# Kernel optimization log

Hardware: AMD Instinct MI355X
Metric: run time of the kernel (lower is better)

Reference implementation:

```python
import jax, jax.numpy as jnp
import numpy as np
from jax import lax

NUM_EMBEDDINGS = 4096
EMBEDDING_DIM = 512
COMMITMENT_COST = 0.1
N_TOKENS = 32768


def setup_inputs() -> dict:
    key = jax.random.key(0)
    kx, kc = jax.random.split(key)
    x = jax.random.normal(kx, (N_TOKENS, EMBEDDING_DIM), dtype=jnp.float32)
    # torch init: uniform_(-1/num_embeddings, 1/num_embeddings)
    lim = 1.0 / NUM_EMBEDDINGS
    codebook = jax.random.uniform(kc, (NUM_EMBEDDINGS, EMBEDDING_DIM),
                                  dtype=jnp.float32, minval=-lim, maxval=lim)
    return {"x": x, "codebook": codebook}


def reference(x, codebook):
    # x: [N, D] (already flat); codebook: [K, D]
    flat = x.reshape(-1, EMBEDDING_DIM)
    distances = (jnp.sum(flat * flat, axis=1, keepdims=True)
                 + jnp.sum(codebook * codebook, axis=1)
                 - 2.0 * jnp.matmul(flat, codebook.T))
    encoding_indices = jnp.argmin(distances, axis=1)  # [N]
    quantized = codebook[encoding_indices].reshape(x.shape)  # gather [N, D]
    e_latent_loss = jnp.mean((lax.stop_gradient(quantized) - x) ** 2)
    q_latent_loss = jnp.mean((quantized - lax.stop_gradient(x)) ** 2)
    loss = q_latent_loss + COMMITMENT_COST * e_latent_loss
    # straight-through estimator
    quantized_st = x + lax.stop_gradient(quantized - x)
    return quantized_st, loss, encoding_indices[:, None]
```

## Files before the change

### kernel.cpp

```cpp
#include <hip/hip_runtime.h>

#define N_TOK 32768
#define DIM 512
#define K_CODES 4096
#define KP 1536
#define CMARG 8e-5f

typedef __attribute__((ext_vector_type(8))) short bf16x8;
typedef __attribute__((ext_vector_type(4))) float f32x4;

__device__ __forceinline__ unsigned short f2bf(float f) {
    unsigned u = __float_as_uint(f);
    return (unsigned short)((u + 0x7FFFu + ((u >> 16) & 1u)) >> 16);
}
__device__ __forceinline__ float bf2f(unsigned short h) {
    return __uint_as_float((unsigned)h << 16);
}
__device__ __forceinline__ void gld16(const void* g, void* l) {
    __builtin_amdgcn_global_load_lds((const __attribute__((address_space(1))) void*)g,
                                     (__attribute__((address_space(3))) void*)l, 16, 0, 0);
}

__global__ __launch_bounds__(256) void vq_x2(const float* __restrict__ X, float* __restrict__ X2) {
    int n = blockIdx.x * 256 + threadIdx.x;
    const float* xr = X + (size_t)n * DIM;
    float blk[4];
    #pragma unroll
    for (int b = 0; b < 4; ++b) {
        const float* p = xr + b * 128;
        float lane[16];
        #pragma unroll
        for (int L = 0; L < 16; ++L) {
            float s[8];
            #pragma unroll
            for (int r = 0; r < 8; ++r) { float x = p[r * 16 + L]; s[r] = __fmul_rn(x, x); }
            float a01 = __fadd_rn(s[0], s[1]);
            float a23 = __fadd_rn(s[2], s[3]);
            float a45 = __fadd_rn(s[4], s[5]);
            float a67 = __fadd_rn(s[6], s[7]);
            lane[L] = __fadd_rn(__fadd_rn(a01, a23), __fadd_rn(a45, a67));
        }
        float t[8];
        #pragma unroll
        for (int L = 0; L < 8; ++L) t[L] = __fadd_rn(lane[L], lane[L + 8]);
        float u[4];
        #pragma unroll
        for (int L = 0; L < 4; ++L) u[L] = __fadd_rn(t[L], t[L + 4]);
        blk[b] = __fadd_rn(__fadd_rn(u[0], u[2]), __fadd_rn(u[1], u[3]));
    }
    X2[n] = __fadd_rn(__fadd_rn(blk[0], blk[1]), __fadd_rn(blk[2], blk[3]));
}

__global__ __launch_bounds__(256) void vq_split(const float* __restrict__ X, const float* __restrict__ CB,
        unsigned short* __restrict__ Ah, unsigned short* __restrict__ Al,
        unsigned short* __restrict__ Eh, unsigned short* __restrict__ El) {
    size_t idx = ((size_t)blockIdx.x * 256 + threadIdx.x) * 8;
    const size_t XE = (size_t)N_TOK * DIM;
    const float* src;
    unsigned short *dh, *dl;
    size_t off;
    if (idx < XE) { src = X + idx; dh = Ah; dl = Al; off = idx; }
    else          { src = CB + (idx - XE); dh = Eh; dl = El; off = idx - XE; }
    float4 v0 = *(const float4*)src;
    float4 v1 = *(const float4*)(src + 4);
    float xv[8] = {v0.x, v0.y, v0.z, v0.w, v1.x, v1.y, v1.z, v1.w};
    union { unsigned short u[8]; uint4 v; } H, L;
    #pragma unroll
    for (int u = 0; u < 8; ++u) {
        unsigned short hb = f2bf(xv[u]);
        H.u[u] = hb;
        L.u[u] = f2bf(__fadd_rn(xv[u], -bf2f(hb)));
    }
    *(uint4*)(dh + off) = H.v;
    *(uint4*)(dl + off) = L.v;
}

__global__ __launch_bounds__(256, 2) void vq_gemm(
        const unsigned short* __restrict__ Ah, const unsigned short* __restrict__ Al,
        const unsigned short* __restrict__ Eh, const unsigned short* __restrict__ El,
        float* __restrict__ Cm, unsigned* __restrict__ Mk) {
    __shared__ __align__(16) unsigned short As[8192];
    __shared__ __align__(16) unsigned short Bs[8192];
    __shared__ float redbuf[2][128];
    __shared__ float tmax[128];
    __shared__ unsigned maskLDS[128][4];

    const int tid = threadIdx.x;
    const int lane = tid & 63;
    const int w = tid >> 6;
    const int wr = w >> 1, wc = w & 1;
    const int bm = blockIdx.x;
    const int bn = blockIdx.y;

    const int srow = tid >> 3;
    const int scol_s = ((tid & 7) * 16) ^ (((tid >> 3) & 7) << 4);

    f32x4 acc[4][4];
    #pragma unroll
    for (int i = 0; i < 4; ++i)
        #pragma unroll
        for (int j = 0; j < 4; ++j) acc[i][j] = (f32x4){0.f, 0.f, 0.f, 0.f};

    const int arow = (lane & 15);
    const int kqb  = (lane >> 4) * 16;

    for (int kt = 0; kt < KP / 64; ++kt) {
        const int kk = kt * 64;
        const int seg = kk >> 9;
        const int kin = kk & 511;
        const unsigned short* Asrc = (seg == 1) ? Al : Ah;
        const unsigned short* Bsrc = (seg == 2) ? El : Eh;
        __syncthreads();
        #pragma unroll
        for (int it = 0; it < 4; ++it) {
            const int row = it * 32 + srow;
            const char* ga = (const char*)Asrc + (size_t)(bm * 128 + row) * 1024 + kin * 2 + scol_s;
            const char* gb = (const char*)Bsrc + (size_t)(bn * 128 + row) * 1024 + kin * 2 + scol_s;
            char* la = (char*)As + it * 4096 + w * 1024;
            char* lb = (char*)Bs + it * 4096 + w * 1024;
            gld16(ga, la);
            gld16(gb, lb);
        }
        asm volatile("s_waitcnt vmcnt(0)" ::: "memory");
        __syncthreads();
        #pragma unroll
        for (int ks = 0; ks < 2; ++ks) {
            bf16x8 a[4], b[4];
            const int kb = ks * 64 + kqb;
            #pragma unroll
            for (int i = 0; i < 4; ++i) {
                int row = wr * 64 + i * 16 + arow;
                a[i] = *(const bf16x8*)((const char*)As + row * 128 + (kb ^ ((row & 7) << 4)));
            }
            #pragma unroll
            for (int j = 0; j < 4; ++j) {
                int row = wc * 64 + j * 16 + arow;
                b[j] = *(const bf16x8*)((const char*)Bs + row * 128 + (kb ^ ((row & 7) << 4)));
            }
            #pragma unroll
            for (int i = 0; i < 4; ++i)
                #pragma unroll
                for (int j = 0; j < 4; ++j)
                    acc[i][j] = __builtin_amdgcn_mfma_f32_16x16x32_bf16(a[i], b[j], acc[i][j], 0, 0, 0);
        }
    }

    float vmax[4][4];
    #pragma unroll
    for (int i = 0; i < 4; ++i)
        #pragma unroll
        for (int r = 0; r < 4; ++r) {
            float m = acc[i][0][r];
            m = fmaxf(m, acc[i][1][r]);
            m = fmaxf(m, acc[i][2][r]);
            m = fmaxf(m, acc[i][3][r]);
            #pragma unroll
            for (int s = 1; s < 16; s <<= 1) m = fmaxf(m, __shfl_xor(m, s));
            vmax[i][r] = m;
        }
    if (tid < 128) { maskLDS[tid][0] = 0; maskLDS[tid][1] = 0; maskLDS[tid][2] = 0; maskLDS[tid][3] = 0; }
    if ((lane & 15) == 0) {
        #pragma unroll
        for (int i = 0; i < 4; ++i)
            #pragma unroll
            for (int r = 0; r < 4; ++r)
                redbuf[wc][wr * 64 + i * 16 + (lane >> 4) * 4 + r] = vmax[i][r];
    }
    __syncthreads();
    if (tid < 128) {
        float tm = fmaxf(redbuf[0][tid], redbuf[1][tid]);
        tmax[tid] = tm;
        Cm[(size_t)(bm * 128 + tid) * 32 + bn] = tm;
    }
    __syncthreads();
    #pragma unroll
    for (int i = 0; i < 4; ++i)
        #pragma unroll
        for (int r = 0; r < 4; ++r) {
            int row = wr * 64 + i * 16 + (lane >> 4) * 4 + r;
            float thr = tmax[row] - CMARG;
            #pragma unroll
            for (int j = 0; j < 4; ++j) {
                if (acc[i][j][r] >= thr) {
                    int col = wc * 64 + j * 16 + (lane & 15);
                    atomicOr(&maskLDS[row][col >> 5], 1u << (col & 31));
                }
            }
        }
    __syncthreads();
    if (tid < 128) {
        uint4 v = make_uint4(maskLDS[tid][0], maskLDS[tid][1], maskLDS[tid][2], maskLDS[tid][3]);
        *(uint4*)&Mk[((size_t)(bm * 128 + tid) * 32 + bn) * 4] = v;
    }
}

__global__ __launch_bounds__(256) void vq_scan(const float* __restrict__ Cm,
        unsigned* __restrict__ list, unsigned* __restrict__ cnt) {
    int n = blockIdx.x * 256 + threadIdx.x;
    const float4* cp = (const float4*)(Cm + (size_t)n * 32);
    float vals[32];
    float m = -3e38f;
    #pragma unroll
    for (int u = 0; u < 8; ++u) {
        float4 v = cp[u];
        vals[u * 4 + 0] = v.x; vals[u * 4 + 1] = v.y; vals[u * 4 + 2] = v.z; vals[u * 4 + 3] = v.w;
        m = fmaxf(m, fmaxf(fmaxf(v.x, v.y), fmaxf(v.z, v.w)));
    }
    float thr = m - CMARG;
    unsigned qm = 0;
    int c = 0;
    #pragma unroll
    for (int t = 0; t < 32; ++t) if (vals[t] >= thr) { qm |= 1u << t; ++c; }
    unsigned pos = atomicAdd(cnt, (unsigned)c);
    while (qm) { int t = __ffs(qm) - 1; qm &= qm - 1; list[pos++] = ((unsigned)n << 5) | (unsigned)t; }
}

__global__ __launch_bounds__(256) void vq_rescore(const float* __restrict__ X, const float* __restrict__ CB,
        const float* __restrict__ X2, const unsigned* __restrict__ Mk,
        const unsigned* __restrict__ list, const unsigned* __restrict__ cnt,
        unsigned long long* __restrict__ best64) {
    const int lw = threadIdx.x >> 6, lane = threadIdx.x & 63;
    unsigned c = *cnt;
    for (unsigned it = blockIdx.x * 4 + lw; it < c; it += gridDim.x * 4) {
        unsigned item = list[it];
        unsigned n = item >> 5, t = item & 31;
        const unsigned* mp = Mk + ((size_t)n * 32 + t) * 4;
        unsigned mw[4] = {mp[0], mp[1], mp[2], mp[3]};
        int nb = __popc(mw[0]) + __popc(mw[1]) + __popc(mw[2]) + __popc(mw[3]);
        const float* xr = X + (size_t)n * DIM;
        float x2 = X2[n];
        unsigned long long bestp = ~0ull;
        for (int base = 0; base < nb; base += 64) {
            int want = base + lane;
            int p = -1;
            if (want < nb) {
                int ww = want;
                #pragma unroll
                for (int wd = 0; wd < 4; ++wd) {
                    int pc = __popc(mw[wd]);
                    if (p < 0) {
                        if (ww < pc) {
                            unsigned mm = mw[wd];
                            for (int z = 0; z < ww; ++z) mm &= mm - 1;
                            p = wd * 32 + __ffs(mm) - 1;
                        } else ww -= pc;
                    }
                }
            }
            int k = (int)(t * 128) + ((p >= 0) ? p : 0);
            const float* er = CB + (size_t)k * DIM;
            float a = 0.f, b = 0.f;
            for (int d = 0; d < 384; ++d) a = fmaf(xr[d], er[d], a);
            for (int d = 384; d < 512; ++d) b = fmaf(xr[d], er[d], b);
            float D = fmaf(-2.f, __fadd_rn(a, b), x2);
            if (p >= 0) {
                unsigned long long pk = ((unsigned long long)__float_as_uint(D) << 32) | (unsigned)k;
                if (pk < bestp) bestp = pk;
            }
        }
        #pragma unroll
        for (int s = 1; s < 64; s <<= 1) {
            unsigned long long o = __shfl_xor(bestp, s);
            if (o < bestp) bestp = o;
        }
        if (lane == 0) atomicMin(best64 + n, bestp);
    }
}

__global__ __launch_bounds__(256) void vq_out2(const float* __restrict__ X,
        const float* __restrict__ CB, const unsigned long long* __restrict__ best64,
        float* __restrict__ outq, float* __restrict__ outidx, float* __restrict__ lossAcc) {
    int tid = threadIdx.x;
    int token = blockIdx.x * 16 + (tid >> 4);
    int chunk = tid & 15;
    unsigned k = (unsigned)(best64[token] & 0xFFFFFFFFull);
    const float4* q4 = (const float4*)(CB + (size_t)k * DIM + chunk * 32);
    const float4* x4 = (const float4*)(X + (size_t)token * DIM + chunk * 32);
    float4* o4 = (float4*)(outq + (size_t)token * DIM + chunk * 32);
    float ls = 0.f;
    #pragma unroll
    for (int u = 0; u < 8; ++u) {
        float4 q = q4[u], xx = x4[u];
        float dx = q.x - xx.x, dy = q.y - xx.y, dz = q.z - xx.z, dw = q.w - xx.w;
        float4 o;
        o.x = xx.x + dx; o.y = xx.y + dy; o.z = xx.z + dz; o.w = xx.w + dw;
        o4[u] = o;
        ls += dx*dx + dy*dy + dz*dz + dw*dw;
    }
    if (chunk == 0) outidx[token] = (float)k;
    #pragma unroll
    for (int s = 1; s < 64; s <<= 1) ls += __shfl_xor(ls, s);
    __shared__ float red[4];
    if ((tid & 63) == 0) red[tid >> 6] = ls;
    __syncthreads();
    if (tid == 0) atomicAdd(lossAcc, red[0] + red[1] + red[2] + red[3]);
}

__global__ void vq_fin(const float* __restrict__ lossAcc, float* __restrict__ outloss) {
    *outloss = 1.1f * (*lossAcc) * (1.0f / 16777216.0f);
}

__global__ __launch_bounds__(256) void vq_np2(const float* __restrict__ X,
        const float* __restrict__ CB, const float* __restrict__ X2,
        unsigned* __restrict__ idxA) {
    __shared__ __align__(16) float es[16][128];
    const int t = threadIdx.x;
    const int ty = t >> 4;
    const int tx = t & 15;
    const int n0 = blockIdx.x * 64;
    const int srow = t >> 1;
    const int scol = (t & 1) * 8;
    const float* xrow0 = X + (size_t)(n0 + ty * 4) * DIM;
    float x2v[4];
    #pragma unroll
    for (int i = 0; i < 4; ++i) x2v[i] = X2[n0 + ty * 4 + i];
    float best[4];
    unsigned bid[4];
    #pragma unroll
    for (int i = 0; i < 4; ++i) { best[i] = 3.0e38f; bid[i] = 0u; }
    float pv[8];
    {
        const float* p = CB + (size_t)srow * DIM + scol;
        *(float4*)&pv[0] = *(const float4*)(p);
        *(float4*)&pv[4] = *(const float4*)(p + 4);
    }
    for (int kt = 0; kt < K_CODES; kt += 128) {
        float accA[4][8], accB[4][8];
        #pragma unroll
        for (int i = 0; i < 4; ++i)
            #pragma unroll
            for (int j = 0; j < 8; ++j) { accA[i][j] = 0.f; accB[i][j] = 0.f; }
        for (int ch = 0; ch < 32; ++ch) {
            const int dt = ch * 16;
            float4 xv[4][4];
            #pragma unroll
            for (int i = 0; i < 4; ++i)
                #pragma unroll
                for (int u = 0; u < 4; ++u)
                    xv[i][u] = *(const float4*)(xrow0 + (size_t)i * DIM + dt + u * 4);
            __syncthreads();
            #pragma unroll
            for (int q = 0; q < 8; ++q) es[scol + q][srow] = pv[q];
            int nkt = kt, nch = ch + 1;
            if (nch == 32) { nch = 0; nkt += 128; }
            if (nkt < K_CODES) {
                const float* p = CB + (size_t)(nkt + srow) * DIM + nch * 16 + scol;
                *(float4*)&pv[0] = *(const float4*)(p);
                *(float4*)&pv[4] = *(const float4*)(p + 4);
            }
            __syncthreads();
            if (ch < 24) {
                #pragma unroll
                for (int d = 0; d < 16; ++d) {
                    const float4 e0 = *(const float4*)&es[d][tx * 4];
                    const float4 e1 = *(const float4*)&es[d][tx * 4 + 64];
                    const float eb[8] = {e0.x, e0.y, e0.z, e0.w, e1.x, e1.y, e1.z, e1.w};
                    #pragma unroll
                    for (int i = 0; i < 4; ++i) {
                        const float xd = ((const float*)&xv[i][0])[d];
                        #pragma unroll
                        for (int j = 0; j < 8; ++j) accA[i][j] = fmaf(xd, eb[j], accA[i][j]);
                    }
                }
            } else {
                #pragma unroll
                for (int d = 0; d < 16; ++d) {
                    const float4 e0 = *(const float4*)&es[d][tx * 4];
                    const float4 e1 = *(const float4*)&es[d][tx * 4 + 64];
                    const float eb[8] = {e0.x, e0.y, e0.z, e0.w, e1.x, e1.y, e1.z, e1.w};
                    #pragma unroll
                    for (int i = 0; i < 4; ++i) {
                        const float xd = ((const float*)&xv[i][0])[d];
                        #pragma unroll
                        for (int j = 0; j < 8; ++j) accB[i][j] = fmaf(xd, eb[j], accB[i][j]);
                    }
                }
            }
        }
        #pragma unroll
        for (int j = 0; j < 8; ++j) {
            const int k = kt + ((j < 4) ? (tx * 4 + j) : (64 + tx * 4 + j - 4));
            #pragma unroll
            for (int i = 0; i < 4; ++i) {
                float C = __fadd_rn(accA[i][j], accB[i][j]);
                float v = fmaf(-2.0f, C, x2v[i]);
                if (v < best[i]) { best[i] = v; bid[i] = (unsigned)k; }
            }
        }
    }
    #pragma unroll
    for (int i = 0; i < 4; ++i) {
        float v = best[i];
        unsigned id = bid[i];
        #pragma unroll
        for (int s = 1; s < 16; s <<= 1) {
            float ov = __shfl_xor(v, s);
            unsigned oid = __shfl_xor(id, s);
            if (ov < v || (ov == v && oid < id)) { v = ov; id = oid; }
        }
        if (tx == 0) idxA[n0 + ty * 4 + i] = id;
    }
}

__global__ __launch_bounds__(256) void vq_out(const float* __restrict__ X,
        const float* __restrict__ CB, const unsigned* __restrict__ idxA,
        float* __restrict__ outq, float* __restrict__ outidx, float* __restrict__ lossAcc) {
    int tid = threadIdx.x;
    int token = blockIdx.x * 16 + (tid >> 4);
    int chunk = tid & 15;
    unsigned k = idxA[token];
    const float4* q4 = (const float4*)(CB + (size_t)k * DIM + chunk * 32);
    const float4* x4 = (const float4*)(X + (size_t)token * DIM + chunk * 32);
    float4* o4 = (float4*)(outq + (size_t)token * DIM + chunk * 32);
    float ls = 0.f;
    #pragma unroll
    for (int u = 0; u < 8; ++u) {
        float4 q = q4[u], xx = x4[u];
        float dx = q.x - xx.x, dy = q.y - xx.y, dz = q.z - xx.z, dw = q.w - xx.w;
        float4 o;
        o.x = xx.x + dx; o.y = xx.y + dy; o.z = xx.z + dz; o.w = xx.w + dw;
        o4[u] = o;
        ls += dx*dx + dy*dy + dz*dz + dw*dw;
    }
    if (chunk == 0) outidx[token] = (float)k;
    #pragma unroll
    for (int s = 1; s < 64; s <<= 1) ls += __shfl_xor(ls, s);
    __shared__ float red[4];
    if ((tid & 63) == 0) red[tid >> 6] = ls;
    __syncthreads();
    if (tid == 0) atomicAdd(lossAcc, red[0] + red[1] + red[2] + red[3]);
}

extern "C" void kernel_launch(void* const* d_in, const int* in_sizes, int n_in,
                              void* d_out, int out_size, void* d_ws, size_t ws_size,
                              hipStream_t stream) {
    const float* X  = (const float*)d_in[0];
    const float* CB = (const float*)d_in[1];
    float* out = (float*)d_out;
    float* outq    = out;
    float* outloss = out + (size_t)N_TOK * DIM;
    float* outidx  = out + (size_t)N_TOK * DIM + 1;

    char* w = (char*)d_ws;
    unsigned* cnt  = (unsigned*)w;
    float* lossAcc = (float*)(w + 4);
    float* X2      = (float*)(w + 256);
    unsigned short* Ah = (unsigned short*)(w + 262144);
    unsigned short* Al = (unsigned short*)(w + 33816576);
    unsigned short* Eh = (unsigned short*)(w + 67371008);
    unsigned short* El = (unsigned short*)(w + 71565312);
    float* Cm          = (float*)(w + 75759616);
    unsigned* Mk       = (unsigned*)(w + 79953920);
    unsigned long long* best64 = (unsigned long long*)(w + 96731136);
    unsigned* list     = (unsigned*)(w + 96993280);
    const size_t WS_NEED = 101187584;

    if (ws_size >= WS_NEED) {
        hipMemsetAsync(d_ws, 0, 64, stream);
        hipMemsetAsync(best64, 0xFF, (size_t)N_TOK * 8, stream);
        vq_x2<<<N_TOK / 256, 256, 0, stream>>>(X, X2);
        vq_split<<<(N_TOK + K_CODES) * DIM / 8 / 256, 256, 0, stream>>>(X, CB, Ah, Al, Eh, El);
        dim3 gg(N_TOK / 128, K_CODES / 128);
        vq_gemm<<<gg, 256, 0, stream>>>(Ah, Al, Eh, El, Cm, Mk);
        vq_scan<<<N_TOK / 256, 256, 0, stream>>>(Cm, list, cnt);
        vq_rescore<<<2048, 256, 0, stream>>>(X, CB, X2, Mk, list, cnt, best64);
        vq_out2<<<N_TOK / 16, 256, 0, stream>>>(X, CB, best64, outq, outidx, lossAcc);
        vq_fin<<<1, 1, 0, stream>>>(lossAcc, outloss);
    } else {
        float* X2f     = (float*)(w + 64);
        unsigned* idxA = (unsigned*)(w + 64 + 131072);
        hipMemsetAsync(d_ws, 0, 64, stream);
        vq_x2<<<N_TOK / 256, 256, 0, stream>>>(X, X2f);
        vq_np2<<<N_TOK / 64, 256, 0, stream>>>(X, CB, X2f, idxA);
        vq_out<<<N_TOK / 16, 256, 0, stream>>>(X, CB, idxA, outq, outidx, lossAcc);
        vq_fin<<<1, 1, 0, stream>>>(lossAcc, outloss);
    }
}
```

Before: 903.4 us.

## Parallelize x-norm kernel, vectorize rescore dot products, raise GEMM occupancy

The squared-norm kernel now splits each token row across four threads with float4 loads and a shuffle reduction. It keeps the same pairwise summation order so the rounding matches. The rescore dot products now use float4 loads with unrolling instead of scalar loops. The GEMM launch bound is raised to request four waves per SIMD, which may force register spills. The fallback path for small workspaces is removed, so the kernel now assumes enough workspace is provided.

```diff
diff --git a/kernel.cpp b/kernel.cpp
--- a/kernel.cpp
+++ b/kernel.cpp
@@ -20,35 +20,49 @@
     __builtin_amdgcn_global_load_lds((const __attribute__((address_space(1))) void*)g,
                                      (__attribute__((address_space(3))) void*)l, 16, 0, 0);
 }
+__device__ __forceinline__ float4 f4add(float4 a, float4 b) {
+    float4 r;
+    r.x = __fadd_rn(a.x, b.x); r.y = __fadd_rn(a.y, b.y);
+    r.z = __fadd_rn(a.z, b.z); r.w = __fadd_rn(a.w, b.w);
+    return r;
+}
 
 __global__ __launch_bounds__(256) void vq_x2(const float* __restrict__ X, float* __restrict__ X2) {
-    int n = blockIdx.x * 256 + threadIdx.x;
-    const float* xr = X + (size_t)n * DIM;
-    float blk[4];
-    #pragma unroll
-    for (int b = 0; b < 4; ++b) {
-        const float* p = xr + b * 128;
-        float lane[16];
-        #pragma unroll
-        for (int L = 0; L < 16; ++L) {
-            float s[8];
-            #pragma unroll
-            for (int r = 0; r < 8; ++r) { float x = p[r * 16 + L]; s[r] = __fmul_rn(x, x); }
-            float a01 = __fadd_rn(s[0], s[1]);
-            float a23 = __fadd_rn(s[2], s[3]);
-            float a45 = __fadd_rn(s[4], s[5]);
-            float a67 = __fadd_rn(s[6], s[7]);
-            lane[L] = __fadd_rn(__fadd_rn(a01, a23), __fadd_rn(a45, a67));
-        }
-        float t[8];
-        #pragma unroll
-        for (int L = 0; L < 8; ++L) t[L] = __fadd_rn(lane[L], lane[L + 8]);
-        float u[4];
-        #pragma unroll
-        for (int L = 0; L < 4; ++L) u[L] = __fadd_rn(t[L], t[L + 4]);
-        blk[b] = __fadd_rn(__fadd_rn(u[0], u[2]), __fadd_rn(u[1], u[3]));
-    }
-    X2[n] = __fadd_rn(__fadd_rn(blk[0], blk[1]), __fadd_rn(blk[2], blk[3]));
+    int gt = blockIdx.x * 256 + threadIdx.x;
+    int n = gt >> 2;
+    int q = gt & 3;
+    const float* p = X + (size_t)n * DIM + q * 128;
+    float4 sq[8][4];
+    #pragma unroll
+    for (int r = 0; r < 8; ++r)
+        #pragma unroll
+        for (int u = 0; u < 4; ++u) {
+            float4 v = *(const float4*)(p + r * 16 + u * 4);
+            float4 s;
+            s.x = __fmul_rn(v.x, v.x); s.y = __fmul_rn(v.y, v.y);
+            s.z = __fmul_rn(v.z, v.z); s.w = __fmul_rn(v.w, v.w);
+            sq[r][u] = s;
+        }
+    float4 lane4[4];
+    #pragma unroll
+    for (int u = 0; u < 4; ++u) {
+        float4 a01 = f4add(sq[0][u], sq[1][u]);
+        float4 a23 = f4add(sq[2][u], sq[3][u]);
+        float4 a45 = f4add(sq[4][u], sq[5][u]);
+        float4 a67 = f4add(sq[6][u], sq[7][u]);
+        lane4[u] = f4add(f4add(a01, a23), f4add(a45, a67));
+    }
+    float4 t0 = f4add(lane4[0], lane4[2]);
+    float4 t1 = f4add(lane4[1], lane4[3]);
+    float4 u4 = f4add(t0, t1);
+    float v0 = __fadd_rn(u4.x, u4.z);
+    float v1 = __fadd_rn(u4.y, u4.w);
+    float blk = __fadd_rn(v0, v1);
+    float o1 = __shfl_xor(blk, 1);
+    float s01 = __fadd_rn(blk, o1);
+    float o2 = __shfl_xor(s01, 2);
+    float tot = __fadd_rn(s01, o2);
+    if (q == 0) X2[n] = tot;
 }
 
 __global__ __launch_bounds__(256) void vq_split(const float* __restrict__ X, const float* __restrict__ CB,
@@ -75,7 +89,7 @@
     *(uint4*)(dl + off) = L.v;
 }
 
-__global__ __launch_bounds__(256, 2) void vq_gemm(
+__global__ __launch_bounds__(256, 4) void vq_gemm(
         const unsigned short* __restrict__ Ah, const unsigned short* __restrict__ Al,
         const unsigned short* __restrict__ Eh, const unsigned short* __restrict__ El,
         float* __restrict__ Cm, unsigned* __restrict__ Mk) {
@@ -250,8 +264,20 @@
             int k = (int)(t * 128) + ((p >= 0) ? p : 0);
             const float* er = CB + (size_t)k * DIM;
             float a = 0.f, b = 0.f;
-            for (int d = 0; d < 384; ++d) a = fmaf(xr[d], er[d], a);
-            for (int d = 384; d < 512; ++d) b = fmaf(xr[d], er[d], b);
+            #pragma unroll 8
+            for (int d4 = 0; d4 < 96; ++d4) {
+                float4 xv = *(const float4*)(xr + d4 * 4);
+                float4 ev = *(const float4*)(er + d4 * 4);
+                a = fmaf(xv.x, ev.x, a); a = fmaf(xv.y, ev.y, a);
+                a = fmaf(xv.z, ev.z, a); a = fmaf(xv.w, ev.w, a);
+            }
+            #pragma unroll 8
+            for (int d4 = 96; d4 < 128; ++d4) {
+                float4 xv = *(const float4*)(xr + d4 * 4);
+                float4 ev = *(const float4*)(er + d4 * 4);
+                b = fmaf(xv.x, ev.x, b); b = fmaf(xv.y, ev.y, b);
+                b = fmaf(xv.z, ev.z, b); b = fmaf(xv.w, ev.w, b);
+            }
             float D = fmaf(-2.f, __fadd_rn(a, b), x2);
             if (p >= 0) {
                 unsigned long long pk = ((unsigned long long)__float_as_uint(D) << 32) | (unsigned)k;
@@ -298,137 +324,6 @@
 
 __global__ void vq_fin(const float* __restrict__ lossAcc, float* __restrict__ outloss) {
     *outloss = 1.1f * (*lossAcc) * (1.0f / 16777216.0f);
-}
-
-__global__ __launch_bounds__(256) void vq_np2(const float* __restrict__ X,
-        const float* __restrict__ CB, const float* __restrict__ X2,
-        unsigned* __restrict__ idxA) {
-    __shared__ __align__(16) float es[16][128];
-    const int t = threadIdx.x;
-    const int ty = t >> 4;
-    const int tx = t & 15;
-    const int n0 = blockIdx.x * 64;
-    const int srow = t >> 1;
-    const int scol = (t & 1) * 8;
-    const float* xrow0 = X + (size_t)(n0 + ty * 4) * DIM;
-    float x2v[4];
-    #pragma unroll
-    for (int i = 0; i < 4; ++i) x2v[i] = X2[n0 + ty * 4 + i];
-    float best[4];
-    unsigned bid[4];
-    #pragma unroll
-    for (int i = 0; i < 4; ++i) { best[i] = 3.0e38f; bid[i] = 0u; }
-    float pv[8];
-    {
-        const float* p = CB + (size_t)srow * DIM + scol;
-        *(float4*)&pv[0] = *(const float4*)(p);
-        *(float4*)&pv[4] = *(const float4*)(p + 4);
-    }
-    for (int kt = 0; kt < K_CODES; kt += 128) {
-        float accA[4][8], accB[4][8];
-        #pragma unroll
-        for (int i = 0; i < 4; ++i)
-            #pragma unroll
-            for (int j = 0; j < 8; ++j) { accA[i][j] = 0.f; accB[i][j] = 0.f; }
-        for (int ch = 0; ch < 32; ++ch) {
-            const int dt = ch * 16;
-            float4 xv[4][4];
-            #pragma unroll
-            for (int i = 0; i < 4; ++i)
-                #pragma unroll
-                for (int u = 0; u < 4; ++u)
-                    xv[i][u] = *(const float4*)(xrow0 + (size_t)i * DIM + dt + u * 4);
-            __syncthreads();
-            #pragma unroll
-            for (int q = 0; q < 8; ++q) es[scol + q][srow] = pv[q];
-            int nkt = kt, nch = ch + 1;
-            if (nch == 32) { nch = 0; nkt += 128; }
-            if (nkt < K_CODES) {
-                const float* p = CB + (size_t)(nkt + srow) * DIM + nch * 16 + scol;
-                *(float4*)&pv[0] = *(const float4*)(p);
-                *(float4*)&pv[4] = *(const float4*)(p + 4);
-            }
-            __syncthreads();
-            if (ch < 24) {
-                #pragma unroll
-                for (int d = 0; d < 16; ++d) {
-                    const float4 e0 = *(const float4*)&es[d][tx * 4];
-                    const float4 e1 = *(const float4*)&es[d][tx * 4 + 64];
-                    const float eb[8] = {e0.x, e0.y, e0.z, e0.w, e1.x, e1.y, e1.z, e1.w};
-                    #pragma unroll
-                    for (int i = 0; i < 4; ++i) {
-                        const float xd = ((const float*)&xv[i][0])[d];
-                        #pragma unroll
-                        for (int j = 0; j < 8; ++j) accA[i][j] = fmaf(xd, eb[j], accA[i][j]);
-                    }
-                }
-            } else {
-                #pragma unroll
-                for (int d = 0; d < 16; ++d) {
-                    const float4 e0 = *(const float4*)&es[d][tx * 4];
-                    const float4 e1 = *(const float4*)&es[d][tx * 4 + 64];
-                    const float eb[8] = {e0.x, e0.y, e0.z, e0.w, e1.x, e1.y, e1.z, e1.w};
-                    #pragma unroll
-                    for (int i = 0; i < 4; ++i) {
-                        const float xd = ((const float*)&xv[i][0])[d];
-                        #pragma unroll
-                        for (int j = 0; j < 8; ++j) accB[i][j] = fmaf(xd, eb[j], accB[i][j]);
-                    }
-                }
-            }
-        }
-        #pragma unroll
-        for (int j = 0; j < 8; ++j) {
-            const int k = kt + ((j < 4) ? (tx * 4 + j) : (64 + tx * 4 + j - 4));
-            #pragma unroll
-            for (int i = 0; i < 4; ++i) {
-                float C = __fadd_rn(accA[i][j], accB[i][j]);
-                float v = fmaf(-2.0f, C, x2v[i]);
-                if (v < best[i]) { best[i] = v; bid[i] = (unsigned)k; }
-            }
-        }
-    }
-    #pragma unroll
-    for (int i = 0; i < 4; ++i) {
-        float v = best[i];
-        unsigned id = bid[i];
-        #pragma unroll
-        for (int s = 1; s < 16; s <<= 1) {
-            float ov = __shfl_xor(v, s);
-            unsigned oid = __shfl_xor(id, s);
-            if (ov < v || (ov == v && oid < id)) { v = ov; id = oid; }
-        }
-        if (tx == 0) idxA[n0 + ty * 4 + i] = id;
-    }
-}
-
-__global__ __launch_bounds__(256) void vq_out(const float* __restrict__ X,
-        const float* __restrict__ CB, const unsigned* __restrict__ idxA,
-        float* __restrict__ outq, float* __restrict__ outidx, float* __restrict__ lossAcc) {
-    int tid = threadIdx.x;
-    int token = blockIdx.x * 16 + (tid >> 4);
-    int chunk = tid & 15;
-    unsigned k = idxA[token];
-    const float4* q4 = (const float4*)(CB + (size_t)k * DIM + chunk * 32);
-    const float4* x4 = (const float4*)(X + (size_t)token * DIM + chunk * 32);
-    float4* o4 = (float4*)(outq + (size_t)token * DIM + chunk * 32);
-    float ls = 0.f;
-    #pragma unroll
-    for (int u = 0; u < 8; ++u) {
-        float4 q = q4[u], xx = x4[u];
-        float dx = q.x - xx.x, dy = q.y - xx.y, dz = q.z - xx.z, dw = q.w - xx.w;
-        float4 o;
-        o.x = xx.x + dx; o.y = xx.y + dy; o.z = xx.z + dz; o.w = xx.w + dw;
-        o4[u] = o;
-        ls += dx*dx + dy*dy + dz*dz + dw*dw;
-    }
-    if (chunk == 0) outidx[token] = (float)k;
-    #pragma unroll
-    for (int s = 1; s < 64; s <<= 1) ls += __shfl_xor(ls, s);
-    __shared__ float red[4];
-    if ((tid & 63) == 0) red[tid >> 6] = ls;
-    __syncthreads();
-    if (tid == 0) atomicAdd(lossAcc, red[0] + red[1] + red[2] + red[3]);
 }
 
 extern "C" void kernel_launch(void* const* d_in, const int* in_sizes, int n_in,
@@ -455,24 +350,15 @@
     unsigned* list     = (unsigned*)(w + 96993280);
     const size_t WS_NEED = 101187584;
 
-    if (ws_size >= WS_NEED) {
-        hipMemsetAsync(d_ws, 0, 64, stream);
-        hipMemsetAsync(best64, 0xFF, (size_t)N_TOK * 8, stream);
-        vq_x2<<<N_TOK / 256, 256, 0, stream>>>(X, X2);
-        vq_split<<<(N_TOK + K_CODES) * DIM / 8 / 256, 256, 0, stream>>>(X, CB, Ah, Al, Eh, El);
-        dim3 gg(N_TOK / 128, K_CODES / 128);
-        vq_gemm<<<gg, 256, 0, stream>>>(Ah, Al, Eh, El, Cm, Mk);
-        vq_scan<<<N_TOK / 256, 256, 0, stream>>>(Cm, list, cnt);
-        vq_rescore<<<2048, 256, 0, stream>>>(X, CB, X2, Mk, list, cnt, best64);
-        vq_out2<<<N_TOK / 16, 256, 0, stream>>>(X, CB, best64, outq, outidx, lossAcc);
-        vq_fin<<<1, 1, 0, stream>>>(lossAcc, outloss);
-    } else {
-        float* X2f     = (float*)(w + 64);
-        unsigned* idxA = (unsigned*)(w + 64 + 131072);
-        hipMemsetAsync(d_ws, 0, 64, stream);
-        vq_x2<<<N_TOK / 256, 256, 0, stream>>>(X, X2f);
-        vq_np2<<<N_TOK / 64, 256, 0, stream>>>(X, CB, X2f, idxA);
-        vq_out<<<N_TOK / 16, 256, 0, stream>>>(X, CB, idxA, outq, outidx, lossAcc);
-        vq_fin<<<1, 1, 0, stream>>>(lossAcc, outloss);
-    }
-}
+    hipMemsetAsync(d_ws, 0, 64, stream);
+    hipMemsetAsync(best64, 0xFF, (size_t)N_TOK * 8, stream);
+    vq_x2<<<N_TOK * 4 / 256, 256, 0, stream>>>(X, X2);
+    vq_split<<<(N_TOK + K_CODES) * DIM / 8 / 256, 256, 0, stream>>>(X, CB, Ah, Al, Eh, El);
+    dim3 gg(N_TOK / 128, K_CODES / 128);
+    vq_gemm<<<gg, 256, 0, stream>>>(Ah, Al, Eh, El, Cm, Mk);
+    vq_scan<<<N_TOK / 256, 256, 0, stream>>>(Cm, list, cnt);
+    vq_rescore<<<2048, 256, 0, stream>>>(X, CB, X2, Mk, list, cnt, best64);
+    vq_out2<<<N_TOK / 16, 256, 0, stream>>>(X, CB, best64, outq, outidx, lossAcc);
+    vq_fin<<<1, 1, 0, stream>>>(lossAcc, outloss);
+    (void)ws_size; (void)WS_NEED;
+}
```

Result: slower. 930.5 us (+3.0%).
